# Kernel tuning notes

Hardware: AMD Instinct MI355X
Metric: run time of the kernel (lower is better)

## Reference

```python
import jax, jax.numpy as jnp
import numpy as np

B, S, H, DH = 8, 2048, 4, 32
D = H * DH  # all_head_size = true_hidden_size = 128


def setup_inputs() -> dict:
    key = jax.random.key(0)
    ks = jax.random.split(key, 9)
    inp = {
        "query_tensor": jax.random.normal(ks[0], (B, S, D), dtype=jnp.float32),
        "key_tensor": jax.random.normal(ks[1], (B, S, D), dtype=jnp.float32),
        "value_tensor": jax.random.normal(ks[2], (B, S, D), dtype=jnp.float32),
        "attention_mask": jnp.zeros((B, 1, 1, S), dtype=jnp.float32),
        "head_mask": jnp.ones((1, H, 1, 1), dtype=jnp.float32),
        "Wq": jax.random.normal(ks[3], (D, D), dtype=jnp.float32) * 0.02,
        "bq": jnp.zeros((D,), dtype=jnp.float32),
        "Wk": jax.random.normal(ks[4], (D, D), dtype=jnp.float32) * 0.02,
        "bk": jnp.zeros((D,), dtype=jnp.float32),
        "Wv": jax.random.normal(ks[5], (D, D), dtype=jnp.float32) * 0.02,
        "bv": jnp.zeros((D,), dtype=jnp.float32),
    }
    return inp


def _split_heads(x):
    # (B, S, D) -> (B, H, S, DH)
    return x.reshape(B, S, H, DH).transpose(0, 2, 1, 3)


def reference(query_tensor, key_tensor, value_tensor, attention_mask, head_mask,
              Wq, bq, Wk, bk, Wv, bv):
    q = _split_heads(query_tensor @ Wq + bq)   # (B,H,S,DH)
    k = _split_heads(key_tensor @ Wk + bk)
    v = _split_heads(value_tensor @ Wv + bv)

    scale = 1.0 / jnp.sqrt(jnp.float32(DH))
    scores = jnp.einsum("bhqd,bhkd->bhqk", q, k) * scale + attention_mask
    probs = jax.nn.softmax(scores, axis=-1)
    # dropout is identity at inference (training=False)
    probs = probs * head_mask
    ctx = jnp.einsum("bhqk,bhkd->bhqd", probs, v)  # (B,H,S,DH)
    ctx = ctx.transpose(0, 2, 1, 3).reshape(B, S, D)
    return ctx
```

## Files before the change

kernel.cpp:

```cpp
#include <hip/hip_runtime.h>
#include <hip/hip_bf16.h>
#include <math.h>

#define B_ 8
#define S_ 2048
#define H_ 4
#define DH_ 32
#define D_ 128
#define BS_ (B_ * S_)
#define LOG2E 1.4426950408889634f
#define QSCALE (0.17677669529663687f * LOG2E)

typedef float f32x4  __attribute__((ext_vector_type(4)));
typedef float f32x16 __attribute__((ext_vector_type(16)));
typedef short s16x8  __attribute__((ext_vector_type(8)));

__device__ __forceinline__ unsigned short bf(float x) {
    return __builtin_bit_cast(unsigned short, __float2bfloat16(x));
}
__device__ __forceinline__ float bf2f(unsigned short u) {
    return __builtin_bit_cast(float, (unsigned int)u << 16);
}
__device__ __forceinline__ unsigned int pk2(float a, float b) {
    unsigned int r;
    asm("v_cvt_pk_bf16_f32 %0, %1, %2" : "=v"(r) : "v"(a), "v"(b));
    return r;
}
__device__ __forceinline__ void pswap(unsigned int& a, unsigned int& b) {
    asm volatile("v_permlane32_swap_b32 %0, %1" : "+v"(a), "+v"(b));
}
__device__ __forceinline__ void gll16(const void* g, void* l) {
    __builtin_amdgcn_global_load_lds(
        (const __attribute__((address_space(1))) unsigned int*)(g),
        (__attribute__((address_space(3))) unsigned int*)(l), 16, 0, 0);
}

#define OFF_Q  0u
#define OFF_K  2097152u
#define OFF_V  4194304u
#define OFF_W  6291456u
#define OFF_E  6389760u

__global__ __launch_bounds__(256) void wprep(
    const float* __restrict__ Wq, const float* __restrict__ Wk, const float* __restrict__ Wv,
    const float* __restrict__ maskg,
    unsigned short* __restrict__ Wt, unsigned short* __restrict__ Em)
{
    if (blockIdx.z == 3) {
        const int id16 = blockIdx.y * 4 + blockIdx.x;
        const int base = id16 * 1024 + threadIdx.x * 4;
        float4 m4 = *(const float4*)&maskg[base];
        ushort4 o;
        o.x = bf(__builtin_amdgcn_exp2f(m4.x * LOG2E));
        o.y = bf(__builtin_amdgcn_exp2f(m4.y * LOG2E));
        o.z = bf(__builtin_amdgcn_exp2f(m4.z * LOG2E));
        o.w = bf(__builtin_amdgcn_exp2f(m4.w * LOG2E));
        *(ushort4*)&Em[base] = o;
        return;
    }
    const float* W = (blockIdx.z == 0) ? Wq : (blockIdx.z == 1) ? Wk : Wv;
    unsigned short* Oh = Wt + (size_t)blockIdx.z * D_ * D_;
    unsigned short* Ol = Oh + 3 * D_ * D_;
    __shared__ float tf[32][36];
    const int t = threadIdx.x;
    const int kt = blockIdx.x * 32, ct = blockIdx.y * 32;
    {
        int kl = t >> 3, cl = (t & 7) * 4;
        float4 w4 = *(const float4*)&W[(size_t)(kt + kl) * D_ + ct + cl];
        tf[kl][cl + 0] = w4.x; tf[kl][cl + 1] = w4.y;
        tf[kl][cl + 2] = w4.z; tf[kl][cl + 3] = w4.w;
    }
    __syncthreads();
    {
        int cl = t >> 3, kl = (t & 7) * 4;
        ushort4 oh, ol;
        float v;
        v = tf[kl + 0][cl]; oh.x = bf(v); ol.x = bf(v - bf2f(oh.x));
        v = tf[kl + 1][cl]; oh.y = bf(v); ol.y = bf(v - bf2f(oh.y));
        v = tf[kl + 2][cl]; oh.z = bf(v); ol.z = bf(v - bf2f(oh.z));
        v = tf[kl + 3][cl]; oh.w = bf(v); ol.w = bf(v - bf2f(oh.w));
        *(ushort4*)&Oh[(size_t)(ct + cl) * D_ + kt + kl] = oh;
        *(ushort4*)&Ol[(size_t)(ct + cl) * D_ + kt + kl] = ol;
    }
}

__global__ __launch_bounds__(256) void qkv_mfma(
    const float* __restrict__ Xq, const float* __restrict__ Xk, const float* __restrict__ Xv,
    const unsigned short* __restrict__ Wt, const float* __restrict__ maskg,
    const float* __restrict__ bq, const float* __restrict__ bk, const float* __restrict__ bv,
    unsigned short* __restrict__ Qo, unsigned short* __restrict__ Kf,
    unsigned short* __restrict__ Vf)
{
    const int mode = blockIdx.z, chalf = blockIdx.y;
    const float* X; const float* bias; float scl;
    if (mode == 0)      { X = Xq; bias = bq; scl = QSCALE; }
    else if (mode == 1) { X = Xk; bias = bk; scl = 1.f; }
    else                { X = Xv; bias = bv; scl = 1.f; }
    const unsigned short* WmH = Wt + (size_t)mode * D_ * D_;
    const unsigned short* WmL = WmH + 3 * D_ * D_;

    __shared__ __align__(16) unsigned short xa[2 * 32 * 136];
    __shared__ __align__(16) unsigned short wt[2 * 64 * 136];

    const int t = threadIdx.x;
    const long row0 = (long)blockIdx.x * 32;

    #pragma unroll
    for (int j = 0; j < 8; j++) {
        int idx = t + 256 * j;
        int part = idx >> 10, i2 = idx & 1023;
        int r = i2 >> 4, c16 = i2 & 15;
        const unsigned short* src = part ? WmL : WmH;
        uint4 v = *(const uint4*)&src[(size_t)(chalf * 64 + r) * D_ + c16 * 8];
        *(uint4*)&wt[part * 8704 + r * 136 + c16 * 8] = v;
    }
    #pragma unroll
    for (int j = 0; j < 4; j++) {
        int idx = t + 256 * j;
        int r = idx >> 5, c4 = idx & 31;
        float4 v = *(const float4*)(X + (row0 + r) * D_ + c4 * 4);
        ushort4 ph, pl;
        ph.x = bf(v.x); pl.x = bf(v.x - bf2f(ph.x));
        ph.y = bf(v.y); pl.y = bf(v.y - bf2f(ph.y));
        ph.z = bf(v.z); pl.z = bf(v.z - bf2f(ph.z));
        ph.w = bf(v.w); pl.w = bf(v.w - bf2f(ph.w));
        *(ushort4*)&xa[r * 136 + c4 * 4] = ph;
        *(ushort4*)&xa[4352 + r * 136 + c4 * 4] = pl;
    }
    __syncthreads();

    const int w = t >> 6, lane = t & 63, lo = lane & 15, hi = lane >> 4;
    const int mf = w >> 1, nb = (w & 1) * 2;
    f32x4 acc[2] = {};
    #pragma unroll
    for (int kk = 0; kk < 4; kk++) {
        const int ko = kk * 32 + hi * 8;
        s16x8 ah = *(const s16x8*)&xa[(mf * 16 + lo) * 136 + ko];
        s16x8 al = *(const s16x8*)&xa[4352 + (mf * 16 + lo) * 136 + ko];
        #pragma unroll
        for (int n2 = 0; n2 < 2; n2++) {
            const int nf = nb + n2;
            s16x8 bh2 = *(const s16x8*)&wt[(nf * 16 + lo) * 136 + ko];
            s16x8 bl2 = *(const s16x8*)&wt[8704 + (nf * 16 + lo) * 136 + ko];
            acc[n2] = __builtin_amdgcn_mfma_f32_16x16x32_bf16(ah, bh2, acc[n2], 0, 0, 0);
            acc[n2] = __builtin_amdgcn_mfma_f32_16x16x32_bf16(al, bh2, acc[n2], 0, 0, 0);
            acc[n2] = __builtin_amdgcn_mfma_f32_16x16x32_bf16(ah, bl2, acc[n2], 0, 0, 0);
        }
    }
    __syncthreads();

    const long b_i = row0 >> 11;
    const long s0g = row0 & 2047;

    if (mode < 2) {
        #pragma unroll
        for (int n2 = 0; n2 < 2; n2++) {
            int c_l = (nb + n2) * 16 + lo;
            float bb = bias[chalf * 64 + c_l];
            #pragma unroll
            for (int r = 0; r < 4; r++) {
                int s = mf * 16 + hi * 4 + r;
                xa[s * 72 + c_l] = bf((acc[n2][r] + bb) * scl);
            }
        }
        __syncthreads();
        int s = t >> 3, part = t & 7;
        int c_g = chalf * 64 + part * 8;
        int h = c_g >> 5, dd = c_g & 31;
        long s_i = s0g + s;
        int bh = (int)(b_i * H_ + h);
        uint4 val = *(const uint4*)&xa[s * 72 + part * 8];
        if (mode == 0) {
            *(uint4*)(Qo + ((size_t)bh * S_ + s_i) * DH_ + dd) = val;
        } else {
            int fr = dd >> 4, hwd = (dd >> 3) & 1;
            size_t off = ((((size_t)bh * 64 + (s_i >> 5)) * 2 + fr) * 64
                          + (s_i & 31) + hwd * 32) * 8;
            *(uint4*)(Kf + off) = val;
        }
    } else {
        float emr[4];
        #pragma unroll
        for (int r = 0; r < 4; r++) {
            const int s_l = mf * 16 + hi * 4 + r;
            emr[r] = __builtin_amdgcn_exp2f(maskg[b_i * S_ + s0g + s_l] * LOG2E);
        }
        #pragma unroll
        for (int n2 = 0; n2 < 2; n2++) {
            int c_l = (nb + n2) * 16 + lo;
            float bb = bias[chalf * 64 + c_l];
            #pragma unroll
            for (int r = 0; r < 4; r++) {
                int s = mf * 16 + hi * 4 + r;
                xa[c_l * 68 + s] = bf((acc[n2][r] + bb) * emr[r]);
            }
        }
        __syncthreads();
        if (t < 128) {
            int c_l = t >> 1, sh2 = (t & 1) * 16;
            int c_g = chalf * 64 + c_l;
            int h = c_g >> 5, dd = c_g & 31;
            long key0 = s0g + sh2;
            int bh = (int)(b_i * H_ + h);
            size_t base = (((size_t)bh * 128 + (key0 >> 4)) * 64 + dd) * 8;
            uint2 p0 = *(const uint2*)&xa[c_l * 68 + sh2 + 0];
            uint2 p1 = *(const uint2*)&xa[c_l * 68 + sh2 + 4];
            uint2 p2 = *(const uint2*)&xa[c_l * 68 + sh2 + 8];
            uint2 p3 = *(const uint2*)&xa[c_l * 68 + sh2 + 12];
            *(uint4*)(Vf + base)       = make_uint4(p0.x, p0.y, p1.x, p1.y);
            *(uint4*)(Vf + base + 256) = make_uint4(p2.x, p2.y, p3.x, p3.y);
        }
    }
}

__global__ __launch_bounds__(512) void flash_mfma(
    const unsigned short* __restrict__ Qg, const unsigned short* __restrict__ Kfg,
    const unsigned short* __restrict__ Vfg, const unsigned short* __restrict__ Emg,
    const float* __restrict__ head_mask, float* __restrict__ Out)
{
    __shared__ __align__(16) unsigned short smem[26624];

    const int t = threadIdx.x, w = t >> 6, lane = t & 63;
    const int l31 = lane & 31, hw = lane >> 5;
    const int kq = w & 3, qh = w >> 2;

    const int lid = blockIdx.x;
    const int xcd = lid & 7, ser = lid >> 3;
    const int bh = xcd * 4 + (ser >> 5);
    const int qi = ser & 31;
    const int b = bh >> 2, h = bh & 3;
    const int q0 = qi * 64 + qh * 32;

    const unsigned short* qp = Qg + ((size_t)bh * S_ + q0 + l31) * DH_ + hw * 8;
    const s16x8 qf0 = *(const s16x8*)qp;
    const s16x8 qf1 = *(const s16x8*)(qp + 16);

    *(uint2*)&smem[24576 + t * 4] = *(const uint2*)(Emg + (size_t)b * S_ + t * 4);

    const size_t kvbase = (size_t)bh * 65536;
    const unsigned short* ksrc = Kfg + kvbase + (size_t)w * 512 + (size_t)lane * 8;
    const unsigned short* vsrc = Vfg + kvbase + (size_t)w * 512 + (size_t)lane * 8;

    gll16(ksrc,        &smem[0 * 4096 + w * 512]);
    gll16(vsrc,        &smem[12288 + 0 * 4096 + w * 512]);
    gll16(ksrc + 4096, &smem[1 * 4096 + w * 512]);
    gll16(vsrc + 4096, &smem[12288 + 1 * 4096 + w * 512]);

    asm volatile("s_waitcnt lgkmcnt(0)" ::: "memory");
    __builtin_amdgcn_sched_barrier(0);

    f32x16 ctx = {}, lacc = {};
    const f32x16 z16 = {};

    for (int tile = 0; tile < 16; tile++) {
        const int cur = tile % 3;

        if (tile < 15) { asm volatile("s_waitcnt vmcnt(2)" ::: "memory"); }
        else           { asm volatile("s_waitcnt vmcnt(0)" ::: "memory"); }
        __builtin_amdgcn_sched_barrier(0);
        __builtin_amdgcn_s_barrier();
        __builtin_amdgcn_sched_barrier(0);

        if (tile < 14) {
            const int pb = (tile + 2) % 3;
            gll16(ksrc + (size_t)(tile + 2) * 4096, &smem[pb * 4096 + w * 512]);
            gll16(vsrc + (size_t)(tile + 2) * 4096, &smem[12288 + pb * 4096 + w * 512]);
        }

        const unsigned short* kb = &smem[cur * 4096 + kq * 1024];
        const unsigned short* vb = &smem[12288 + cur * 4096 + kq * 1024];
        const s16x8 kf0 = *(const s16x8*)(kb + (size_t)lane * 8);
        const s16x8 kf1 = *(const s16x8*)(kb + 512 + (size_t)lane * 8);
        const s16x8 vf0 = *(const s16x8*)(vb + (size_t)lane * 8);
        const s16x8 vf1 = *(const s16x8*)(vb + 512 + (size_t)lane * 8);
        const s16x8 ef0 = *(const s16x8*)&smem[24576 + tile * 128 + kq * 32 + hw * 8];
        const s16x8 ef1 = *(const s16x8*)&smem[24576 + tile * 128 + kq * 32 + hw * 8 + 16];

        __builtin_amdgcn_s_setprio(1);
        f32x16 s = __builtin_amdgcn_mfma_f32_32x32x16_bf16(kf0, qf0, z16, 0, 0, 0);
        s = __builtin_amdgcn_mfma_f32_32x32x16_bf16(kf1, qf1, s, 0, 0, 0);
        __builtin_amdgcn_s_setprio(0);

        unsigned int pd[8];
        #pragma unroll
        for (int j = 0; j < 8; j++) {
            const float p0 = __builtin_amdgcn_exp2f(s[2 * j]);
            const float p1 = __builtin_amdgcn_exp2f(s[2 * j + 1]);
            pd[j] = pk2(p0, p1);
        }
        pswap(pd[0], pd[2]); pswap(pd[1], pd[3]);
        pswap(pd[4], pd[6]); pswap(pd[5], pd[7]);
        const s16x8 pa0 = __builtin_bit_cast(s16x8, make_uint4(pd[0], pd[1], pd[2], pd[3]));
        const s16x8 pa1 = __builtin_bit_cast(s16x8, make_uint4(pd[4], pd[5], pd[6], pd[7]));

        __builtin_amdgcn_s_setprio(1);
        ctx  = __builtin_amdgcn_mfma_f32_32x32x16_bf16(pa0, vf0, ctx, 0, 0, 0);
        lacc = __builtin_amdgcn_mfma_f32_32x32x16_bf16(pa0, ef0, lacc, 0, 0, 0);
        ctx  = __builtin_amdgcn_mfma_f32_32x32x16_bf16(pa1, vf1, ctx, 0, 0, 0);
        lacc = __builtin_amdgcn_mfma_f32_32x32x16_bf16(pa1, ef1, lacc, 0, 0, 0);
        __builtin_amdgcn_s_setprio(0);
    }

    __syncthreads();
    float* ms = (float*)smem;
    #define MS(qh_, sl_, ln_, r_) ms[(((qh_) * 2 + (sl_)) * 64 + (ln_)) * 33 + (r_)]

    if (kq >= 2) {
        #pragma unroll
        for (int r = 0; r < 16; r++) {
            MS(qh, kq - 2, lane, r) = ctx[r];
            MS(qh, kq - 2, lane, 16 + r) = lacc[r];
        }
    }
    __syncthreads();
    if (kq < 2) {
        #pragma unroll
        for (int r = 0; r < 16; r++) {
            ctx[r]  += MS(qh, kq, lane, r);
            lacc[r] += MS(qh, kq, lane, 16 + r);
        }
    }
    __syncthreads();
    if (kq == 1) {
        #pragma unroll
        for (int r = 0; r < 16; r++) {
            MS(qh, 0, lane, r) = ctx[r];
            MS(qh, 0, lane, 16 + r) = lacc[r];
        }
    }
    __syncthreads();
    if (kq == 0) {
        #pragma unroll
        for (int r = 0; r < 16; r++) {
            ctx[r]  += MS(qh, 0, lane, r);
            lacc[r] += MS(qh, 0, lane, 16 + r);
        }
        const float hm = head_mask[h];
        #pragma unroll
        for (int r = 0; r < 16; r++) {
            const int qrow = (r & 3) + 8 * (r >> 2) + 4 * hw;
            Out[((size_t)b * S_ + q0 + qrow) * D_ + h * DH_ + l31] = ctx[r] * hm / lacc[r];
        }
    }
    #undef MS
}

extern "C" void kernel_launch(void* const* d_in, const int* in_sizes, int n_in,
                              void* d_out, int out_size, void* d_ws, size_t ws_size,
                              hipStream_t stream) {
    const float* Xq   = (const float*)d_in[0];
    const float* Xk   = (const float*)d_in[1];
    const float* Xv   = (const float*)d_in[2];
    const float* mask = (const float*)d_in[3];
    const float* hm   = (const float*)d_in[4];
    const float* Wq   = (const float*)d_in[5];
    const float* bq   = (const float*)d_in[6];
    const float* Wk   = (const float*)d_in[7];
    const float* bk   = (const float*)d_in[8];
    const float* Wv   = (const float*)d_in[9];
    const float* bv   = (const float*)d_in[10];
    float* out = (float*)d_out;

    unsigned short* ws = (unsigned short*)d_ws;
    unsigned short* Qo = ws + OFF_Q;
    unsigned short* Kf = ws + OFF_K;
    unsigned short* Vf = ws + OFF_V;
    unsigned short* Wt = ws + OFF_W;
    unsigned short* Em = ws + OFF_E;

    wprep<<<dim3(4, 4, 4), 256, 0, stream>>>(Wq, Wk, Wv, mask, Wt, Em);
    qkv_mfma<<<dim3(BS_ / 32, 2, 3), 256, 0, stream>>>(Xq, Xk, Xv, Wt, mask,
                                                       bq, bk, bv, Qo, Kf, Vf);
    flash_mfma<<<dim3(1024), 512, 0, stream>>>(Qo, Kf, Vf, Em, hm, out);
}
```

Baseline: 55.37 us.

## Give each wave private double-buffered KV slices and drop per-tile block barriers

The flash kernel now has each wave load its own K/V slice into a private double-buffered shared-memory region. This removes the workgroup-wide s_barrier on every tile, and the triple-buffered cooperative load is replaced by per-wave waits on vmcnt and lgkmcnt. Each K/V slice is now loaded redundantly by the two waves sharing a kq, which raises global/L2 traffic and grows the LDS footprint. Separately, the QKV projection kernel drops its weight staging in LDS and reads weight fragments straight from global memory.

After: 73.34 us. +32.5%, slower.

```diff
diff --git a/kernel.cpp b/kernel.cpp
--- a/kernel.cpp
+++ b/kernel.cpp
@@ -100,20 +100,10 @@
     const unsigned short* WmL = WmH + 3 * D_ * D_;
 
     __shared__ __align__(16) unsigned short xa[2 * 32 * 136];
-    __shared__ __align__(16) unsigned short wt[2 * 64 * 136];
 
     const int t = threadIdx.x;
     const long row0 = (long)blockIdx.x * 32;
 
-    #pragma unroll
-    for (int j = 0; j < 8; j++) {
-        int idx = t + 256 * j;
-        int part = idx >> 10, i2 = idx & 1023;
-        int r = i2 >> 4, c16 = i2 & 15;
-        const unsigned short* src = part ? WmL : WmH;
-        uint4 v = *(const uint4*)&src[(size_t)(chalf * 64 + r) * D_ + c16 * 8];
-        *(uint4*)&wt[part * 8704 + r * 136 + c16 * 8] = v;
-    }
     #pragma unroll
     for (int j = 0; j < 4; j++) {
         int idx = t + 256 * j;
@@ -140,8 +130,9 @@
         #pragma unroll
         for (int n2 = 0; n2 < 2; n2++) {
             const int nf = nb + n2;
-            s16x8 bh2 = *(const s16x8*)&wt[(nf * 16 + lo) * 136 + ko];
-            s16x8 bl2 = *(const s16x8*)&wt[8704 + (nf * 16 + lo) * 136 + ko];
+            const size_t wrow = (size_t)(chalf * 64 + nf * 16 + lo) * D_ + ko;
+            s16x8 bh2 = *(const s16x8*)&WmH[wrow];
+            s16x8 bl2 = *(const s16x8*)&WmL[wrow];
             acc[n2] = __builtin_amdgcn_mfma_f32_16x16x32_bf16(ah, bh2, acc[n2], 0, 0, 0);
             acc[n2] = __builtin_amdgcn_mfma_f32_16x16x32_bf16(al, bh2, acc[n2], 0, 0, 0);
             acc[n2] = __builtin_amdgcn_mfma_f32_16x16x32_bf16(ah, bl2, acc[n2], 0, 0, 0);
@@ -218,7 +209,7 @@
     const unsigned short* __restrict__ Vfg, const unsigned short* __restrict__ Emg,
     const float* __restrict__ head_mask, float* __restrict__ Out)
 {
-    __shared__ __align__(16) unsigned short smem[26624];
+    __shared__ __align__(16) unsigned short smem[34816];
 
     const int t = threadIdx.x, w = t >> 6, lane = t & 63;
     const int l31 = lane & 31, hw = lane >> 5;
@@ -235,46 +226,53 @@
     const s16x8 qf0 = *(const s16x8*)qp;
     const s16x8 qf1 = *(const s16x8*)(qp + 16);
 
-    *(uint2*)&smem[24576 + t * 4] = *(const uint2*)(Emg + (size_t)b * S_ + t * 4);
+    *(uint2*)&smem[32768 + t * 4] = *(const uint2*)(Emg + (size_t)b * S_ + t * 4);
 
     const size_t kvbase = (size_t)bh * 65536;
-    const unsigned short* ksrc = Kfg + kvbase + (size_t)w * 512 + (size_t)lane * 8;
-    const unsigned short* vsrc = Vfg + kvbase + (size_t)w * 512 + (size_t)lane * 8;
-
-    gll16(ksrc,        &smem[0 * 4096 + w * 512]);
-    gll16(vsrc,        &smem[12288 + 0 * 4096 + w * 512]);
-    gll16(ksrc + 4096, &smem[1 * 4096 + w * 512]);
-    gll16(vsrc + 4096, &smem[12288 + 1 * 4096 + w * 512]);
-
-    asm volatile("s_waitcnt lgkmcnt(0)" ::: "memory");
-    __builtin_amdgcn_sched_barrier(0);
+    const unsigned short* ksrc = Kfg + kvbase + (size_t)kq * 1024 + (size_t)lane * 8;
+    const unsigned short* vsrc = Vfg + kvbase + (size_t)kq * 1024 + (size_t)lane * 8;
+    unsigned short* reg0 = &smem[w * 4096];
+    unsigned short* reg1 = &smem[w * 4096 + 2048];
+
+    {
+        gll16(ksrc,              reg0);
+        gll16(ksrc + 512,        reg0 + 512);
+        gll16(vsrc,              reg0 + 1024);
+        gll16(vsrc + 512,        reg0 + 1536);
+        gll16(ksrc + 4096,       reg1);
+        gll16(ksrc + 4096 + 512, reg1 + 512);
+        gll16(vsrc + 4096,       reg1 + 1024);
+        gll16(vsrc + 4096 + 512, reg1 + 1536);
+    }
+    __syncthreads();
 
     f32x16 ctx = {}, lacc = {};
     const f32x16 z16 = {};
 
     for (int tile = 0; tile < 16; tile++) {
-        const int cur = tile % 3;
-
-        if (tile < 15) { asm volatile("s_waitcnt vmcnt(2)" ::: "memory"); }
+        unsigned short* cur = (tile & 1) ? reg1 : reg0;
+
+        if (tile < 15) { asm volatile("s_waitcnt vmcnt(4)" ::: "memory"); }
         else           { asm volatile("s_waitcnt vmcnt(0)" ::: "memory"); }
         __builtin_amdgcn_sched_barrier(0);
-        __builtin_amdgcn_s_barrier();
+
+        const s16x8 kf0 = *(const s16x8*)(cur + (size_t)lane * 8);
+        const s16x8 kf1 = *(const s16x8*)(cur + 512 + (size_t)lane * 8);
+        const s16x8 vf0 = *(const s16x8*)(cur + 1024 + (size_t)lane * 8);
+        const s16x8 vf1 = *(const s16x8*)(cur + 1536 + (size_t)lane * 8);
+        const s16x8 ef0 = *(const s16x8*)&smem[32768 + tile * 128 + kq * 32 + hw * 8];
+        const s16x8 ef1 = *(const s16x8*)&smem[32768 + tile * 128 + kq * 32 + hw * 8 + 16];
+
+        asm volatile("s_waitcnt lgkmcnt(0)" ::: "memory");
         __builtin_amdgcn_sched_barrier(0);
-
         if (tile < 14) {
-            const int pb = (tile + 2) % 3;
-            gll16(ksrc + (size_t)(tile + 2) * 4096, &smem[pb * 4096 + w * 512]);
-            gll16(vsrc + (size_t)(tile + 2) * 4096, &smem[12288 + pb * 4096 + w * 512]);
-        }
-
-        const unsigned short* kb = &smem[cur * 4096 + kq * 1024];
-        const unsigned short* vb = &smem[12288 + cur * 4096 + kq * 1024];
-        const s16x8 kf0 = *(const s16x8*)(kb + (size_t)lane * 8);
-        const s16x8 kf1 = *(const s16x8*)(kb + 512 + (size_t)lane * 8);
-        const s16x8 vf0 = *(const s16x8*)(vb + (size_t)lane * 8);
-        const s16x8 vf1 = *(const s16x8*)(vb + 512 + (size_t)lane * 8);
-        const s16x8 ef0 = *(const s16x8*)&smem[24576 + tile * 128 + kq * 32 + hw * 8];
-        const s16x8 ef1 = *(const s16x8*)&smem[24576 + tile * 128 + kq * 32 + hw * 8 + 16];
+            const unsigned short* kp2 = ksrc + (size_t)(tile + 2) * 4096;
+            const unsigned short* vp2 = vsrc + (size_t)(tile + 2) * 4096;
+            gll16(kp2,       cur);
+            gll16(kp2 + 512, cur + 512);
+            gll16(vp2,       cur + 1024);
+            gll16(vp2 + 512, cur + 1536);
+        }
 
         __builtin_amdgcn_s_setprio(1);
         f32x16 s = __builtin_amdgcn_mfma_f32_32x32x16_bf16(kf0, qf0, z16, 0, 0, 0);
```

## Software-pipeline QK^T of next tile against softmax/PV of current tile

Applied to the files above, without the earlier changes.

Restructures the attention inner loop so the QK^T MFMAs and LDS fragment loads for tile t+1 are issued before the exp2 and PV MFMAs of tile t. This lets the transcendental work overlap with matrix-core work. The prefetch depth also grows from two to three K/V tiles in flight, and the loop is fully unrolled with the setprio hints removed. In exchange it raises register pressure from the extra live fragments, and its barrier and wait-count ordering is more delicate.

After: 54.13 us. 2.2% less time.

```diff
diff --git a/kernel.cpp b/kernel.cpp
--- a/kernel.cpp
+++ b/kernel.cpp
@@ -231,74 +231,92 @@
     const int b = bh >> 2, h = bh & 3;
     const int q0 = qi * 64 + qh * 32;
 
+    *(uint2*)&smem[24576 + t * 4] = *(const uint2*)(Emg + (size_t)b * S_ + t * 4);
+
     const unsigned short* qp = Qg + ((size_t)bh * S_ + q0 + l31) * DH_ + hw * 8;
     const s16x8 qf0 = *(const s16x8*)qp;
     const s16x8 qf1 = *(const s16x8*)(qp + 16);
 
-    *(uint2*)&smem[24576 + t * 4] = *(const uint2*)(Emg + (size_t)b * S_ + t * 4);
-
     const size_t kvbase = (size_t)bh * 65536;
     const unsigned short* ksrc = Kfg + kvbase + (size_t)w * 512 + (size_t)lane * 8;
     const unsigned short* vsrc = Vfg + kvbase + (size_t)w * 512 + (size_t)lane * 8;
 
-    gll16(ksrc,        &smem[0 * 4096 + w * 512]);
-    gll16(vsrc,        &smem[12288 + 0 * 4096 + w * 512]);
-    gll16(ksrc + 4096, &smem[1 * 4096 + w * 512]);
-    gll16(vsrc + 4096, &smem[12288 + 1 * 4096 + w * 512]);
-
-    asm volatile("s_waitcnt lgkmcnt(0)" ::: "memory");
-    __builtin_amdgcn_sched_barrier(0);
-
+    #pragma unroll
+    for (int p = 0; p < 3; p++) {
+        gll16(ksrc + (size_t)p * 4096, &smem[p * 4096 + w * 512]);
+        gll16(vsrc + (size_t)p * 4096, &smem[12288 + p * 4096 + w * 512]);
+    }
+    __syncthreads();
+
+    const unsigned short* emb = &smem[24576];
     f32x16 ctx = {}, lacc = {};
     const f32x16 z16 = {};
 
+    s16x8 vf_cur0, vf_cur1, ef_cur0, ef_cur1;
+    f32x16 s_cur;
+    {
+        const unsigned short* kb = &smem[kq * 1024];
+        const unsigned short* vb = &smem[12288 + kq * 1024];
+        s16x8 k0 = *(const s16x8*)(kb + (size_t)lane * 8);
+        s16x8 k1 = *(const s16x8*)(kb + 512 + (size_t)lane * 8);
+        vf_cur0 = *(const s16x8*)(vb + (size_t)lane * 8);
+        vf_cur1 = *(const s16x8*)(vb + 512 + (size_t)lane * 8);
+        ef_cur0 = *(const s16x8*)(emb + kq * 32 + hw * 8);
+        ef_cur1 = *(const s16x8*)(emb + kq * 32 + hw * 8 + 16);
+        s_cur = __builtin_amdgcn_mfma_f32_32x32x16_bf16(k0, qf0, z16, 0, 0, 0);
+        s_cur = __builtin_amdgcn_mfma_f32_32x32x16_bf16(k1, qf1, s_cur, 0, 0, 0);
+    }
+
+    #pragma unroll
     for (int tile = 0; tile < 16; tile++) {
-        const int cur = tile % 3;
-
-        if (tile < 15) { asm volatile("s_waitcnt vmcnt(2)" ::: "memory"); }
-        else           { asm volatile("s_waitcnt vmcnt(0)" ::: "memory"); }
+        if (tile < 14)       { asm volatile("s_waitcnt vmcnt(2)" ::: "memory"); }
+        else if (tile == 14) { asm volatile("s_waitcnt vmcnt(0)" ::: "memory"); }
         __builtin_amdgcn_sched_barrier(0);
         __builtin_amdgcn_s_barrier();
         __builtin_amdgcn_sched_barrier(0);
 
-        if (tile < 14) {
-            const int pb = (tile + 2) % 3;
-            gll16(ksrc + (size_t)(tile + 2) * 4096, &smem[pb * 4096 + w * 512]);
-            gll16(vsrc + (size_t)(tile + 2) * 4096, &smem[12288 + pb * 4096 + w * 512]);
-        }
-
-        const unsigned short* kb = &smem[cur * 4096 + kq * 1024];
-        const unsigned short* vb = &smem[12288 + cur * 4096 + kq * 1024];
-        const s16x8 kf0 = *(const s16x8*)(kb + (size_t)lane * 8);
-        const s16x8 kf1 = *(const s16x8*)(kb + 512 + (size_t)lane * 8);
-        const s16x8 vf0 = *(const s16x8*)(vb + (size_t)lane * 8);
-        const s16x8 vf1 = *(const s16x8*)(vb + 512 + (size_t)lane * 8);
-        const s16x8 ef0 = *(const s16x8*)&smem[24576 + tile * 128 + kq * 32 + hw * 8];
-        const s16x8 ef1 = *(const s16x8*)&smem[24576 + tile * 128 + kq * 32 + hw * 8 + 16];
-
-        __builtin_amdgcn_s_setprio(1);
-        f32x16 s = __builtin_amdgcn_mfma_f32_32x32x16_bf16(kf0, qf0, z16, 0, 0, 0);
-        s = __builtin_amdgcn_mfma_f32_32x32x16_bf16(kf1, qf1, s, 0, 0, 0);
-        __builtin_amdgcn_s_setprio(0);
+        f32x16 s_next;
+        s16x8 vf_n0, vf_n1, ef_n0, ef_n1;
+        if (tile < 15) {
+            const int nb3 = ((tile + 1) % 3) * 4096 + kq * 1024;
+            const unsigned short* kb = &smem[nb3];
+            const unsigned short* vb = &smem[12288 + nb3];
+            s16x8 kn0 = *(const s16x8*)(kb + (size_t)lane * 8);
+            s16x8 kn1 = *(const s16x8*)(kb + 512 + (size_t)lane * 8);
+            vf_n0 = *(const s16x8*)(vb + (size_t)lane * 8);
+            vf_n1 = *(const s16x8*)(vb + 512 + (size_t)lane * 8);
+            ef_n0 = *(const s16x8*)(emb + (tile + 1) * 128 + kq * 32 + hw * 8);
+            ef_n1 = *(const s16x8*)(emb + (tile + 1) * 128 + kq * 32 + hw * 8 + 16);
+            s_next = __builtin_amdgcn_mfma_f32_32x32x16_bf16(kn0, qf0, z16, 0, 0, 0);
+            s_next = __builtin_amdgcn_mfma_f32_32x32x16_bf16(kn1, qf1, s_next, 0, 0, 0);
+
+            if (tile <= 12) {
+                gll16(ksrc + (size_t)(tile + 3) * 4096, &smem[(tile % 3) * 4096 + w * 512]);
+                gll16(vsrc + (size_t)(tile + 3) * 4096, &smem[12288 + (tile % 3) * 4096 + w * 512]);
+            }
+        }
 
         unsigned int pd[8];
         #pragma unroll
         for (int j = 0; j < 8; j++) {
-            const float p0 = __builtin_amdgcn_exp2f(s[2 * j]);
-            const float p1 = __builtin_amdgcn_exp2f(s[2 * j + 1]);
-            pd[j] = pk2(p0, p1);
+            pd[j] = pk2(__builtin_amdgcn_exp2f(s_cur[2 * j]),
+                        __builtin_amdgcn_exp2f(s_cur[2 * j + 1]));
         }
         pswap(pd[0], pd[2]); pswap(pd[1], pd[3]);
         pswap(pd[4], pd[6]); pswap(pd[5], pd[7]);
         const s16x8 pa0 = __builtin_bit_cast(s16x8, make_uint4(pd[0], pd[1], pd[2], pd[3]));
         const s16x8 pa1 = __builtin_bit_cast(s16x8, make_uint4(pd[4], pd[5], pd[6], pd[7]));
 
-        __builtin_amdgcn_s_setprio(1);
-        ctx  = __builtin_amdgcn_mfma_f32_32x32x16_bf16(pa0, vf0, ctx, 0, 0, 0);
-        lacc = __builtin_amdgcn_mfma_f32_32x32x16_bf16(pa0, ef0, lacc, 0, 0, 0);
-        ctx  = __builtin_amdgcn_mfma_f32_32x32x16_bf16(pa1, vf1, ctx, 0, 0, 0);
-        lacc = __builtin_amdgcn_mfma_f32_32x32x16_bf16(pa1, ef1, lacc, 0, 0, 0);
-        __builtin_amdgcn_s_setprio(0);
+        ctx  = __builtin_amdgcn_mfma_f32_32x32x16_bf16(pa0, vf_cur0, ctx, 0, 0, 0);
+        lacc = __builtin_amdgcn_mfma_f32_32x32x16_bf16(pa0, ef_cur0, lacc, 0, 0, 0);
+        ctx  = __builtin_amdgcn_mfma_f32_32x32x16_bf16(pa1, vf_cur1, ctx, 0, 0, 0);
+        lacc = __builtin_amdgcn_mfma_f32_32x32x16_bf16(pa1, ef_cur1, lacc, 0, 0, 0);
+
+        if (tile < 15) {
+            s_cur = s_next;
+            vf_cur0 = vf_n0; vf_cur1 = vf_n1;
+            ef_cur0 = ef_n0; ef_cur1 = ef_n1;
+        }
     }
 
     __syncthreads();
```
